# Optimization experiments

Hardware: AMD Instinct MI355X
Metric: run time of the kernel (lower is better)

The kernel has to match this reference:

```python
import jax, jax.numpy as jnp
import numpy as np
from jax import lax

N, D, NUM_SPEC, NUM_HOPS = 8192, 256, 32, 3
ETA, EPS, LN_EPS = 0.5, 0.5, 1e-5


def setup_inputs() -> dict:
    key = jax.random.key(0)
    ks = jax.random.split(key, 4)
    H = jax.random.normal(ks[0], (N, D), dtype=jnp.float32)
    # normalized adjacency proxy: scale so spectral norm is O(1) and hops stay stable
    A = jax.random.normal(ks[1], (N, N), dtype=jnp.float32) / jnp.sqrt(jnp.float32(N))
    # orthonormal-ish eigenvector columns
    V = jax.random.normal(ks[2], (N, NUM_SPEC), dtype=jnp.float32)
    V = V / jnp.linalg.norm(V, axis=0, keepdims=True)
    eigvals = jax.random.uniform(ks[3], (NUM_SPEC,), dtype=jnp.float32, maxval=2.0)
    return {
        "H": H,
        "A": A,
        "V": V,
        "eigvals": eigvals,
        "spec_logits": jnp.zeros((NUM_SPEC,), jnp.float32),
        "lap_logits": jnp.full((NUM_SPEC,), 0.1, jnp.float32),
        "hop_weights": jnp.full((NUM_HOPS + 1,), 1.0 / (NUM_HOPS + 1), jnp.float32),
        "threshold": jnp.full((D,), 0.05, jnp.float32),
        "ln_gamma": jnp.ones((D,), jnp.float32),
        "ln_beta": jnp.zeros((D,), jnp.float32),
    }


def reference(H, A, V, eigvals, spec_logits, lap_logits, hop_weights, threshold, ln_gamma, ln_beta):
    n, d = H.shape
    num_hops = hop_weights.shape[0] - 1

    # hop propagation: hops[k] = A^k H, shape [K, n, d] with K = num_hops+1
    def step(Hc, _):
        Hn = A @ Hc
        return Hn, Hn
    _, rest = lax.scan(step, H, None, length=num_hops)
    hops = jnp.concatenate([H[None], rest], axis=0)  # [K, n, d]

    hop_w = jax.nn.softmax(hop_weights)          # [K]
    spec_w = jax.nn.softmax(spec_logits)         # [S]
    lap_lams = jax.nn.softplus(lap_logits)       # [S]
    coeff = jnp.float32(d) / (jnp.float32(n) * jnp.float32(EPS) ** 2)

    # Phi[k,s,:] = v_s^T H_k  -> batched rank-1 projections
    Phi = jnp.einsum('ns,knd->ksd', V, hops)     # [K, S, d]

    # M = I + coeff * phi phi^T, batched small [d,d] SPD solves
    eye = jnp.eye(d, dtype=H.dtype)
    M = eye + coeff * jnp.einsum('ksi,ksj->ksij', Phi, Phi)  # [K,S,d,d]
    # phi @ M^{-1} == M^{-1} phi (M symmetric)
    q = coeff * jnp.linalg.solve(M, Phi[..., None])[..., 0]  # [K,S,d]

    # grad_R_total = sum_{k,s} hop_w[k] spec_w[s] v_s q_{k,s}^T = V @ T_R
    T_R = spec_w[:, None] * jnp.einsum('k,ksd->sd', hop_w, q)       # [S,d]
    grad_R = V @ T_R                                                 # [n,d]

    # grad_L_total = sum_{k,s} hop_w[k] lap_lams[s] eig_s v_s phi_{k,s}^T
    T_L = (lap_lams * eigvals)[:, None] * jnp.einsum('k,ksd->sd', hop_w, Phi)
    grad_L = V @ T_L

    H_half = H + ETA * grad_R - ETA * grad_L

    # soft threshold (proximal L1)
    thr = threshold[None, :]
    H_out = jnp.sign(H_half) * jax.nn.relu(jnp.abs(H_half) - thr)

    # LayerNorm over last dim
    mu = jnp.mean(H_out, axis=-1, keepdims=True)
    var = jnp.var(H_out, axis=-1, keepdims=True)
    H_out = (H_out - mu) / jnp.sqrt(var + LN_EPS) * ln_gamma + ln_beta
    return (H_out, lax.stop_gradient(hop_w), lax.stop_gradient(spec_w))
```

## Files before the change

### kernel.cpp

```cpp
#include <hip/hip_runtime.h>
#include <stdint.h>

#define NN 8192
#define DIM 256
#define NSPEC 32
#define ZSPLIT 32
#define MCH (NN / ZSPLIT)
#define ETA 0.5f
#define COEFF 0.125f
#define LNEPS 1e-5f

__launch_bounds__(256, 4)
__global__ void gemm_ATW(const float* __restrict__ A, const float* __restrict__ W,
                         float* __restrict__ P) {
    __shared__ float ldsW[MCH * NSPEC];
    const int t = threadIdx.x;
    const int w = t >> 6, l = t & 63;
    const long n0 = (long)blockIdx.x * 256;
    const int  m0 = blockIdx.y * MCH;

#pragma unroll
    for (int i = 0; i < 8; ++i) {
        int idx = i * 256 + t;
        *(float4*)&ldsW[idx * 4] = *(const float4*)&W[(long)m0 * NSPEC + idx * 4];
    }
    __syncthreads();

    float acc[4][8];
#pragma unroll
    for (int j = 0; j < 4; ++j)
#pragma unroll
        for (int k = 0; k < 8; ++k) acc[j][k] = 0.f;

    const float* Arow = A + (long)m0 * NN + n0 + l * 4;
    const float* wrow = ldsW + w * 8;
#pragma unroll 4
    for (int im = 0; im < MCH; ++im) {
        float4 a4 = *(const float4*)(Arow + (long)im * NN);
        float4 w0 = *(const float4*)(wrow + im * NSPEC);
        float4 w1 = *(const float4*)(wrow + im * NSPEC + 4);
        float a[4]  = {a4.x, a4.y, a4.z, a4.w};
        float ww[8] = {w0.x, w0.y, w0.z, w0.w, w1.x, w1.y, w1.z, w1.w};
#pragma unroll
        for (int j = 0; j < 4; ++j)
#pragma unroll
            for (int k = 0; k < 8; ++k)
                acc[j][k] += a[j] * ww[k];
    }

    float* Pp = P + ((n0 + l * 4) * ZSPLIT + blockIdx.y) * NSPEC + w * 8;
#pragma unroll
    for (int j = 0; j < 4; ++j) {
        float4 o0 = {acc[j][0], acc[j][1], acc[j][2], acc[j][3]};
        float4 o1 = {acc[j][4], acc[j][5], acc[j][6], acc[j][7]};
        *(float4*)&Pp[(long)j * ZSPLIT * NSPEC] = o0;
        *(float4*)&Pp[(long)j * ZSPLIT * NSPEC + 4] = o1;
    }
}

__global__ void reduce32(const float* __restrict__ P, float* __restrict__ Wf) {
    int t = threadIdx.x;
    long n = (long)blockIdx.x * 8 + (t >> 5);
    int s = t & 31;
    const float* p = P + n * (ZSPLIT * NSPEC) + s;
    float v = 0.f;
#pragma unroll
    for (int z = 0; z < ZSPLIT; ++z) v += p[z * NSPEC];
    Wf[n * NSPEC + s] = v;
}

__global__ void phi_kernel(const float* __restrict__ W0, const float* __restrict__ W1,
                           const float* __restrict__ W2, const float* __restrict__ W3,
                           const float* __restrict__ H, float* __restrict__ Phi) {
    __shared__ float ldsW[64 * NSPEC];
    int t = threadIdx.x;
    int s0 = (t >> 6) * 8;
    int d0 = (t & 63) * 4;
    int n0 = blockIdx.x * 128;
    int k = blockIdx.y;
    const float* W = (k == 0) ? W0 : (k == 1) ? W1 : (k == 2) ? W2 : W3;
    float4 acc[8];
#pragma unroll
    for (int j = 0; j < 8; ++j) acc[j] = (float4){0.f, 0.f, 0.f, 0.f};

    for (int tile = 0; tile < 2; ++tile) {
        int nb = n0 + tile * 64;
#pragma unroll
        for (int i = 0; i < 8; ++i) {
            int idx = i * 256 + t;
            ldsW[idx] = W[(long)(nb + (idx >> 5)) * NSPEC + (idx & 31)];
        }
        __syncthreads();
        for (int nn = 0; nn < 64; ++nn) {
            float4 x = *(const float4*)&H[(long)(nb + nn) * DIM + d0];
#pragma unroll
            for (int j = 0; j < 8; ++j) {
                float vs = ldsW[nn * NSPEC + s0 + j];
                acc[j].x += vs * x.x; acc[j].y += vs * x.y;
                acc[j].z += vs * x.z; acc[j].w += vs * x.w;
            }
        }
        __syncthreads();
    }
#pragma unroll
    for (int j = 0; j < 8; ++j) {
        float* ph = &Phi[((k * NSPEC) + s0 + j) * DIM + d0];
        atomicAdd(ph + 0, acc[j].x);
        atomicAdd(ph + 1, acc[j].y);
        atomicAdd(ph + 2, acc[j].z);
        atomicAdd(ph + 3, acc[j].w);
    }
}

__global__ void tc_kernel(const float* __restrict__ Phi,
                          const float* __restrict__ eigvals,
                          const float* __restrict__ spec_logits,
                          const float* __restrict__ lap_logits,
                          const float* __restrict__ hop_weights,
                          float* __restrict__ Tc,
                          float* __restrict__ out_tail) {
    int s = blockIdx.x, t = threadIdx.x;
    float hw0 = hop_weights[0], hw1 = hop_weights[1], hw2 = hop_weights[2], hw3 = hop_weights[3];
    float hm = fmaxf(fmaxf(hw0, hw1), fmaxf(hw2, hw3));
    hw0 = expf(hw0 - hm); hw1 = expf(hw1 - hm); hw2 = expf(hw2 - hm); hw3 = expf(hw3 - hm);
    float hs = hw0 + hw1 + hw2 + hw3;
    hw0 /= hs; hw1 /= hs; hw2 /= hs; hw3 /= hs;
    float hw[4] = {hw0, hw1, hw2, hw3};
    float sm = -1e30f;
    for (int j = 0; j < NSPEC; ++j) sm = fmaxf(sm, spec_logits[j]);
    float ssum = 0.f;
    for (int j = 0; j < NSPEC; ++j) ssum += expf(spec_logits[j] - sm);
    float spec_w_s = expf(spec_logits[s] - sm) / ssum;
    float lp = lap_logits[s];
    float lap = (lp > 20.f) ? lp : log1pf(expf(lp));
    float le = lap * eigvals[s];

    __shared__ float red[4];
    float accR = 0.f, accL = 0.f;
    for (int k = 0; k < 4; ++k) {
        float phi = Phi[(k * NSPEC + s) * DIM + t];
        float v = phi * phi;
        for (int off = 32; off; off >>= 1) v += __shfl_xor(v, off);
        if ((t & 63) == 0) red[t >> 6] = v;
        __syncthreads();
        float ssq = red[0] + red[1] + red[2] + red[3];
        __syncthreads();
        float q = COEFF * phi / (1.f + COEFF * ssq);
        accR += hw[k] * q;
        accL += hw[k] * phi;
    }
    Tc[s * DIM + t] = spec_w_s * accR - le * accL;
    if (s == 0) {
        if (t < 4) out_tail[t] = hw[t];
        if (t < NSPEC) out_tail[4 + t] = expf(spec_logits[t] - sm) / ssum;
    }
}

__launch_bounds__(256)
__global__ void final_kernel(const float* __restrict__ H, const float* __restrict__ V,
                             const float* __restrict__ Tc, const float* __restrict__ thr,
                             const float* __restrict__ gamma, const float* __restrict__ beta,
                             float* __restrict__ out) {
    __shared__ float tc[NSPEC * DIM];
    int t = threadIdx.x;
    {
        const float4* s4 = (const float4*)Tc;
        float4* d4 = (float4*)tc;
        for (int i = 0; i < 8; ++i) d4[i * 256 + t] = s4[i * 256 + t];
    }
    __syncthreads();
    int w = t >> 6, l = t & 63;
    long row = (long)blockIdx.x * 4 + w;
    int d0 = l * 4;
    const float* vrow = V + row * NSPEC;
    float4 G = {0.f, 0.f, 0.f, 0.f};
#pragma unroll 8
    for (int s = 0; s < NSPEC; ++s) {
        float vs = vrow[s];
        float4 c4 = *(const float4*)&tc[s * DIM + d0];
        G.x += vs * c4.x; G.y += vs * c4.y; G.z += vs * c4.z; G.w += vs * c4.w;
    }
    float4 h = *(const float4*)&H[row * DIM + d0];
    float4 th = *(const float4*)&thr[d0];
    float y[4];
    y[0] = h.x + ETA * G.x; y[1] = h.y + ETA * G.y;
    y[2] = h.z + ETA * G.z; y[3] = h.w + ETA * G.w;
    float tv[4] = {th.x, th.y, th.z, th.w};
    float s1 = 0.f, s2 = 0.f;
#pragma unroll
    for (int j = 0; j < 4; ++j) {
        float a = fabsf(y[j]) - tv[j];
        y[j] = (a > 0.f) ? copysignf(a, y[j]) : 0.f;
        s1 += y[j];
        s2 += y[j] * y[j];
    }
    for (int off = 32; off; off >>= 1) { s1 += __shfl_xor(s1, off); s2 += __shfl_xor(s2, off); }
    float mean = s1 * (1.f / DIM);
    float var = s2 * (1.f / DIM) - mean * mean;
    float inv = rsqrtf(var + LNEPS);
    float4 g4 = *(const float4*)&gamma[d0];
    float4 b4 = *(const float4*)&beta[d0];
    float4 o;
    o.x = (y[0] - mean) * inv * g4.x + b4.x;
    o.y = (y[1] - mean) * inv * g4.y + b4.y;
    o.z = (y[2] - mean) * inv * g4.z + b4.z;
    o.w = (y[3] - mean) * inv * g4.w + b4.w;
    *(float4*)&out[row * DIM + d0] = o;
}

extern "C" void kernel_launch(void* const* d_in, const int* in_sizes, int n_in,
                              void* d_out, int out_size, void* d_ws, size_t ws_size,
                              hipStream_t stream) {
    const float* H = (const float*)d_in[0];
    const float* A = (const float*)d_in[1];
    const float* V = (const float*)d_in[2];
    const float* eigvals = (const float*)d_in[3];
    const float* spec_logits = (const float*)d_in[4];
    const float* lap_logits = (const float*)d_in[5];
    const float* hop_weights = (const float*)d_in[6];
    const float* threshold = (const float*)d_in[7];
    const float* ln_gamma = (const float*)d_in[8];
    const float* ln_beta = (const float*)d_in[9];

    char* ws = (char*)d_ws;
    float* P   = (float*)ws;
    float* W1f = (float*)(ws + 33554432);
    float* W2f = (float*)(ws + 34603008);
    float* W3f = (float*)(ws + 35651584);
    float* Phi = (float*)(ws + 36700160);
    float* Tc  = (float*)(ws + 36831232);
    float* out = (float*)d_out;

    hipMemsetAsync(Phi, 0, 4 * NSPEC * DIM * sizeof(float), stream);

    gemm_ATW<<<dim3(32, ZSPLIT), 256, 0, stream>>>(A, V, P);
    reduce32<<<1024, 256, 0, stream>>>(P, W1f);
    gemm_ATW<<<dim3(32, ZSPLIT), 256, 0, stream>>>(A, W1f, P);
    reduce32<<<1024, 256, 0, stream>>>(P, W2f);
    gemm_ATW<<<dim3(32, ZSPLIT), 256, 0, stream>>>(A, W2f, P);
    reduce32<<<1024, 256, 0, stream>>>(P, W3f);

    phi_kernel<<<dim3(64, 4), 256, 0, stream>>>(V, W1f, W2f, W3f, H, Phi);
    tc_kernel<<<NSPEC, 256, 0, stream>>>(Phi, eigvals, spec_logits, lap_logits, hop_weights,
                                         Tc, out + (long)NN * DIM);
    final_kernel<<<2048, 256, 0, stream>>>(H, V, Tc, threshold, ln_gamma, ln_beta, out);
}
```

Before: 643.2 us.

## Compute hop powers directly with bf16 MFMA GEMMs instead of fp32 A^T V chains

Replaces the transposed-propagation scheme (A^T applied to 32-column V with split-K and reductions) with explicit propagation A^k H using bf16 MFMA matrix cores. A is cast to padded bf16 once, and H is transposed to bf16 for the B operand. Each hop writes bf16 and fp32 copies, and phi is then computed from V and the hop features. This uses matrix cores but performs far more arithmetic and loses precision through bf16 across three hops.

New measurement: 1.338 ms. 108% more time.

```diff
diff --git a/kernel.cpp b/kernel.cpp
--- a/kernel.cpp
+++ b/kernel.cpp
@@ -1,84 +1,136 @@
 #include <hip/hip_runtime.h>
+#include <hip/hip_bf16.h>
 #include <stdint.h>
 
 #define NN 8192
+#define LDA 8320
+#define LDU 8320
 #define DIM 256
 #define NSPEC 32
-#define ZSPLIT 32
-#define MCH (NN / ZSPLIT)
 #define ETA 0.5f
 #define COEFF 0.125f
 #define LNEPS 1e-5f
-
-__launch_bounds__(256, 4)
-__global__ void gemm_ATW(const float* __restrict__ A, const float* __restrict__ W,
-                         float* __restrict__ P) {
-    __shared__ float ldsW[MCH * NSPEC];
+#define KSTEPS (NN / 32)
+
+typedef __attribute__((ext_vector_type(8))) short bf16x8;
+typedef __attribute__((ext_vector_type(4))) float f32x4;
+typedef __attribute__((ext_vector_type(4))) unsigned short u16x4;
+
+__device__ __forceinline__ unsigned short bf2u(__hip_bfloat16 b) {
+    union { __hip_bfloat16 b; unsigned short u; } c; c.b = b; return c.u;
+}
+
+__global__ void cast_A(const float* __restrict__ A, __hip_bfloat16* __restrict__ Ab) {
+    const long row = blockIdx.x;
+    const float* src = A + row * NN;
+    __hip_bfloat16* dst = Ab + row * LDA;
     const int t = threadIdx.x;
-    const int w = t >> 6, l = t & 63;
-    const long n0 = (long)blockIdx.x * 256;
-    const int  m0 = blockIdx.y * MCH;
-
-#pragma unroll
-    for (int i = 0; i < 8; ++i) {
+#pragma unroll
+    for (int i = 0; i < 4; ++i) {
+        int base = (i * 256 + t) * 8;
+        float4 v0 = *(const float4*)(src + base);
+        float4 v1 = *(const float4*)(src + base + 4);
+        unsigned short pk[8];
+        pk[0] = bf2u(__float2bfloat16(v0.x)); pk[1] = bf2u(__float2bfloat16(v0.y));
+        pk[2] = bf2u(__float2bfloat16(v0.z)); pk[3] = bf2u(__float2bfloat16(v0.w));
+        pk[4] = bf2u(__float2bfloat16(v1.x)); pk[5] = bf2u(__float2bfloat16(v1.y));
+        pk[6] = bf2u(__float2bfloat16(v1.z)); pk[7] = bf2u(__float2bfloat16(v1.w));
+        *(bf16x8*)(dst + base) = *(bf16x8*)pk;
+    }
+}
+
+__global__ void transH(const float* __restrict__ H, __hip_bfloat16* __restrict__ UT0) {
+    __shared__ float lds[64 * 260];
+    const int t = threadIdx.x;
+    const int n0 = blockIdx.x * 64;
+#pragma unroll
+    for (int i = 0; i < 16; ++i) {
         int idx = i * 256 + t;
-        *(float4*)&ldsW[idx * 4] = *(const float4*)&W[(long)m0 * NSPEC + idx * 4];
+        int n = idx >> 6, c = idx & 63;
+        float4 v = *(const float4*)&H[(long)(n0 + n) * DIM + c * 4];
+        lds[n * 260 + c * 4 + 0] = v.x; lds[n * 260 + c * 4 + 1] = v.y;
+        lds[n * 260 + c * 4 + 2] = v.z; lds[n * 260 + c * 4 + 3] = v.w;
     }
     __syncthreads();
-
-    float acc[4][8];
-#pragma unroll
-    for (int j = 0; j < 4; ++j)
-#pragma unroll
-        for (int k = 0; k < 8; ++k) acc[j][k] = 0.f;
-
-    const float* Arow = A + (long)m0 * NN + n0 + l * 4;
-    const float* wrow = ldsW + w * 8;
+#pragma unroll
+    for (int j = 0; j < 8; ++j) {
+        int idx = j * 256 + t;
+        int d = idx >> 3, g = idx & 7;
+        unsigned short pk[8];
+#pragma unroll
+        for (int e = 0; e < 8; ++e)
+            pk[e] = bf2u(__float2bfloat16(lds[(g * 8 + e) * 260 + d]));
+        *(bf16x8*)&UT0[(long)d * LDU + n0 + g * 8] = *(bf16x8*)pk;
+    }
+}
+
+__launch_bounds__(512, 2)
+__global__ void hop(const __hip_bfloat16* __restrict__ Ab,
+                    const __hip_bfloat16* __restrict__ UTin,
+                    __hip_bfloat16* __restrict__ UTout,
+                    float* __restrict__ Ufout) {
+    const int t = threadIdx.x;
+    const int wv = t >> 6, l = t & 63;
+    const int wm = wv & 1;
+    const int wd = (wv >> 1) * 64;
+    const int lr = l & 15;
+    const int lk = (l >> 4) * 8;
+    const long m0 = (long)blockIdx.x * 32 + wm * 16;
+
+    const __hip_bfloat16* Ap = Ab + (m0 + lr) * (long)LDA + lk;
+    const __hip_bfloat16* Bp = UTin + (long)(wd + lr) * LDU + lk;
+
+    f32x4 acc[4];
+#pragma unroll
+    for (int dt = 0; dt < 4; ++dt) acc[dt] = (f32x4){0.f, 0.f, 0.f, 0.f};
+
+    bf16x8 af[4];
+    bf16x8 bfr[4][4];
+#pragma unroll
+    for (int p = 0; p < 4; ++p) {
+        af[p] = *(const bf16x8*)(Ap + p * 32);
+#pragma unroll
+        for (int dt = 0; dt < 4; ++dt)
+            bfr[p][dt] = *(const bf16x8*)(Bp + (long)dt * 16 * LDU + p * 32);
+    }
+
 #pragma unroll 4
-    for (int im = 0; im < MCH; ++im) {
-        float4 a4 = *(const float4*)(Arow + (long)im * NN);
-        float4 w0 = *(const float4*)(wrow + im * NSPEC);
-        float4 w1 = *(const float4*)(wrow + im * NSPEC + 4);
-        float a[4]  = {a4.x, a4.y, a4.z, a4.w};
-        float ww[8] = {w0.x, w0.y, w0.z, w0.w, w1.x, w1.y, w1.z, w1.w};
-#pragma unroll
-        for (int j = 0; j < 4; ++j)
-#pragma unroll
-            for (int k = 0; k < 8; ++k)
-                acc[j][k] += a[j] * ww[k];
-    }
-
-    float* Pp = P + ((n0 + l * 4) * ZSPLIT + blockIdx.y) * NSPEC + w * 8;
-#pragma unroll
-    for (int j = 0; j < 4; ++j) {
-        float4 o0 = {acc[j][0], acc[j][1], acc[j][2], acc[j][3]};
-        float4 o1 = {acc[j][4], acc[j][5], acc[j][6], acc[j][7]};
-        *(float4*)&Pp[(long)j * ZSPLIT * NSPEC] = o0;
-        *(float4*)&Pp[(long)j * ZSPLIT * NSPEC + 4] = o1;
-    }
-}
-
-__global__ void reduce32(const float* __restrict__ P, float* __restrict__ Wf) {
-    int t = threadIdx.x;
-    long n = (long)blockIdx.x * 8 + (t >> 5);
-    int s = t & 31;
-    const float* p = P + n * (ZSPLIT * NSPEC) + s;
-    float v = 0.f;
-#pragma unroll
-    for (int z = 0; z < ZSPLIT; ++z) v += p[z * NSPEC];
-    Wf[n * NSPEC + s] = v;
-}
-
-__global__ void phi_kernel(const float* __restrict__ W0, const float* __restrict__ W1,
-                           const float* __restrict__ W2, const float* __restrict__ W3,
-                           const float* __restrict__ H, float* __restrict__ Phi) {
+    for (int kk = 0; kk < KSTEPS; ++kk) {
+        const int cur = kk & 3;
+#pragma unroll
+        for (int dt = 0; dt < 4; ++dt)
+            acc[dt] = __builtin_amdgcn_mfma_f32_16x16x32_bf16(af[cur], bfr[cur][dt],
+                                                              acc[dt], 0, 0, 0);
+        if (kk + 4 < KSTEPS) {
+            af[cur] = *(const bf16x8*)(Ap + (kk + 4) * 32);
+#pragma unroll
+            for (int dt = 0; dt < 4; ++dt)
+                bfr[cur][dt] = *(const bf16x8*)(Bp + (long)dt * 16 * LDU + (kk + 4) * 32);
+        }
+    }
+
+#pragma unroll
+    for (int dt = 0; dt < 4; ++dt) {
+        const int d = wd + dt * 16 + lr;
+#pragma unroll
+        for (int r = 0; r < 4; ++r) {
+            const long m = m0 + (l >> 4) * 4 + r;
+            UTout[(long)d * LDU + m] = __float2bfloat16(acc[dt][r]);
+            Ufout[m * (long)DIM + d] = acc[dt][r];
+        }
+    }
+}
+
+__global__ void phi_kernel(const float* __restrict__ V, const float* __restrict__ H0,
+                           const float* __restrict__ U1, const float* __restrict__ U2,
+                           const float* __restrict__ U3, float* __restrict__ Phi) {
     __shared__ float ldsW[64 * NSPEC];
     int t = threadIdx.x;
     int s0 = (t >> 6) * 8;
     int d0 = (t & 63) * 4;
     int n0 = blockIdx.x * 128;
     int k = blockIdx.y;
-    const float* W = (k == 0) ? W0 : (k == 1) ? W1 : (k == 2) ? W2 : W3;
+    const float* Hk = (k == 0) ? H0 : (k == 1) ? U1 : (k == 2) ? U2 : U3;
     float4 acc[8];
 #pragma unroll
     for (int j = 0; j < 8; ++j) acc[j] = (float4){0.f, 0.f, 0.f, 0.f};
@@ -88,11 +140,11 @@
 #pragma unroll
         for (int i = 0; i < 8; ++i) {
             int idx = i * 256 + t;
-            ldsW[idx] = W[(long)(nb + (idx >> 5)) * NSPEC + (idx & 31)];
+            ldsW[idx] = V[(long)(nb + (idx >> 5)) * NSPEC + (idx & 31)];
         }
         __syncthreads();
         for (int nn = 0; nn < 64; ++nn) {
-            float4 x = *(const float4*)&H[(long)(nb + nn) * DIM + d0];
+            float4 x = *(const float4*)&Hk[(long)(nb + nn) * DIM + d0];
 #pragma unroll
             for (int j = 0; j < 8; ++j) {
                 float vs = ldsW[nn * NSPEC + s0 + j];
@@ -223,24 +275,28 @@
     const float* ln_beta = (const float*)d_in[9];
 
     char* ws = (char*)d_ws;
-    float* P   = (float*)ws;
-    float* W1f = (float*)(ws + 33554432);
-    float* W2f = (float*)(ws + 34603008);
-    float* W3f = (float*)(ws + 35651584);
-    float* Phi = (float*)(ws + 36700160);
-    float* Tc  = (float*)(ws + 36831232);
+    __hip_bfloat16* Ab  = (__hip_bfloat16*)ws;
+    __hip_bfloat16* UT0 = (__hip_bfloat16*)(ws + 136314880);
+    __hip_bfloat16* UT1 = (__hip_bfloat16*)(ws + 140574720);
+    __hip_bfloat16* UT2 = (__hip_bfloat16*)(ws + 144834560);
+    __hip_bfloat16* UT3 = (__hip_bfloat16*)(ws + 149094400);
+    float* Uf1 = (float*)(ws + 153354240);
+    float* Uf2 = (float*)(ws + 161742848);
+    float* Uf3 = (float*)(ws + 170131456);
+    float* Phi = (float*)(ws + 178520064);
+    float* Tc  = (float*)(ws + 178651136);
     float* out = (float*)d_out;
 
     hipMemsetAsync(Phi, 0, 4 * NSPEC * DIM * sizeof(float), stream);
 
-    gemm_ATW<<<dim3(32, ZSPLIT), 256, 0, stream>>>(A, V, P);
-    reduce32<<<1024, 256, 0, stream>>>(P, W1f);
-    gemm_ATW<<<dim3(32, ZSPLIT), 256, 0, stream>>>(A, W1f, P);
-    reduce32<<<1024, 256, 0, stream>>>(P, W2f);
-    gemm_ATW<<<dim3(32, ZSPLIT), 256, 0, stream>>>(A, W2f, P);
-    reduce32<<<1024, 256, 0, stream>>>(P, W3f);
-
-    phi_kernel<<<dim3(64, 4), 256, 0, stream>>>(V, W1f, W2f, W3f, H, Phi);
+    cast_A<<<8192, 256, 0, stream>>>(A, Ab);
+    transH<<<128, 256, 0, stream>>>(H, UT0);
+
+    hop<<<256, 512, 0, stream>>>(Ab, UT0, UT1, Uf1);
+    hop<<<256, 512, 0, stream>>>(Ab, UT1, UT2, Uf2);
+    hop<<<256, 512, 0, stream>>>(Ab, UT2, UT3, Uf3);
+
+    phi_kernel<<<dim3(64, 4), 256, 0, stream>>>(V, H, Uf1, Uf2, Uf3, Phi);
     tc_kernel<<<NSPEC, 256, 0, stream>>>(Phi, eigvals, spec_logits, lap_logits, hop_weights,
                                          Tc, out + (long)NN * DIM);
     final_kernel<<<2048, 256, 0, stream>>>(H, V, Tc, threshold, ln_gamma, ln_beta, out);
```
